# Kernel optimization log

Measured on AMD Instinct MI355X. Metric: run time of the kernel, lower is better.

## Reference

```python
import jax, jax.numpy as jnp
import numpy as np

N_NODES = 100000
N_EDGES = 1600000
IN_DIM = 128
HID_DIM = 64
OUT_DIM = 1


def setup_inputs() -> dict:
    key = jax.random.key(0)
    k = jax.random.split(key, 8)
    x = jax.random.normal(k[0], (N_NODES, IN_DIM), dtype=jnp.float32)
    edge_index = jax.random.randint(k[1], (2, N_EDGES), 0, N_NODES, dtype=jnp.int64)
    # GCNConv layer 1: weight [IN, HID], bias [HID] (glorot-ish scale)
    W1 = jax.random.normal(k[2], (IN_DIM, HID_DIM), dtype=jnp.float32) / np.sqrt(IN_DIM)
    b1 = jnp.zeros((HID_DIM,), dtype=jnp.float32)
    W2 = jax.random.normal(k[3], (HID_DIM, HID_DIM), dtype=jnp.float32) / np.sqrt(HID_DIM)
    b2 = jnp.zeros((HID_DIM,), dtype=jnp.float32)
    Wfc = jax.random.normal(k[4], (HID_DIM, OUT_DIM), dtype=jnp.float32) / np.sqrt(HID_DIM)
    bfc = jnp.zeros((OUT_DIM,), dtype=jnp.float32)
    return {"x": x, "edge_index": edge_index, "W1": W1, "b1": b1,
            "W2": W2, "b2": b2, "Wfc": Wfc, "bfc": bfc}


def _gcn_norm(edge_index, n_nodes):
    # PyG GCNConv default: add self-loops, symmetric normalization.
    src, dst = edge_index[0], edge_index[1]
    loop = jnp.arange(n_nodes, dtype=src.dtype)
    src = jnp.concatenate([src, loop])
    dst = jnp.concatenate([dst, loop])
    deg = jax.ops.segment_sum(jnp.ones_like(dst, dtype=jnp.float32), dst,
                              num_segments=n_nodes)
    deg_isqrt = jax.lax.rsqrt(deg)  # deg >= 1 thanks to self-loops
    norm = deg_isqrt[src] * deg_isqrt[dst]  # [E+N]
    return src, dst, norm


def _gcn_conv(x, src, dst, norm, W, b, n_nodes):
    h = x @ W                      # [N, D_out] dense transform first (D_out <= D_in)
    msg = h[src] * norm[:, None]   # gather + normalize  [E+N, D_out]
    out = jax.ops.segment_sum(msg, dst, num_segments=n_nodes)  # scatter-add
    return out + b


def reference(x, edge_index, W1, b1, W2, b2, Wfc, bfc):
    n = x.shape[0]
    src, dst, norm = _gcn_norm(edge_index, n)
    h = jax.nn.relu(_gcn_conv(x, src, dst, norm, W1, b1, n))
    h = jax.nn.relu(_gcn_conv(h, src, dst, norm, W2, b2, n))
    return h @ Wfc + bfc  # [N, 1]
```

## Files before the change

kernel.cpp:

```cpp
#include <hip/hip_runtime.h>
#include <hip/hip_bf16.h>


#define IN_DIM 128
#define HID 64
#define B1 256
#define MAXNC 128

typedef unsigned int uint;

__device__ inline uint pack_bf16x2(float a, float b) {
    uint ua = __builtin_bit_cast(uint, a);
    uint ub = __builtin_bit_cast(uint, b);
    ua += 0x7fffu + ((ua >> 16) & 1u);
    ub += 0x7fffu + ((ub >> 16) & 1u);
    return (ua >> 16) | (ub & 0xffff0000u);
}
__device__ inline float bf_lo(uint g) { return __builtin_bit_cast(float, g << 16); }
__device__ inline float bf_hi(uint g) { return __builtin_bit_cast(float, g & 0xffff0000u); }

__global__ __launch_bounds__(512) void hist1(const int* __restrict__ dst,
                                             int* __restrict__ ghist,
                                             int E, int NC, int chunk) {
    __shared__ int h[MAXNC];
    int t = threadIdx.x, blk = blockIdx.x;
    if (t < NC) h[t] = 0;
    __syncthreads();
    int s = blk * chunk, e = min(E, s + chunk);
    for (int i = s + t; i < e; i += 512) atomicAdd(&h[dst[i] >> 10], 1);
    __syncthreads();
    if (t < NC) ghist[(size_t)t * B1 + blk] = h[t];
}

__global__ __launch_bounds__(1024) void scan_mat(int* __restrict__ a, int M,
                                                 int* __restrict__ row_off, int N) {
    __shared__ int ws[16], wsoff[16], total_s;
    int t = threadIdx.x;
    int seg = (M + 1023) >> 10;
    int s = t * seg, e = min(M, s + seg);
    int sum = 0;
    for (int i = s; i < e; ++i) sum += a[i];
    int incl = sum;
#pragma unroll
    for (int o = 1; o < 64; o <<= 1) {
        int u = __shfl_up(incl, o, 64);
        if ((t & 63) >= o) incl += u;
    }
    if ((t & 63) == 63) ws[t >> 6] = incl;
    __syncthreads();
    if (t == 0) {
        int run = 0;
#pragma unroll
        for (int i = 0; i < 16; ++i) { wsoff[i] = run; run += ws[i]; }
        total_s = run;
    }
    __syncthreads();
    int run = wsoff[t >> 6] + incl - sum;
    for (int i = s; i < e; ++i) { int tmp = a[i]; a[i] = run; run += tmp; }
    if (t == 0) row_off[N] = total_s;
}

__global__ __launch_bounds__(512) void scatter1(const int* __restrict__ src,
                                                const int* __restrict__ dst,
                                                const int* __restrict__ goff,
                                                uint* __restrict__ pairs,
                                                int E, int NC, int chunk) {
    __shared__ int cur[MAXNC];
    int t = threadIdx.x, blk = blockIdx.x;
    if (t < NC) cur[t] = goff[(size_t)t * B1 + blk];
    __syncthreads();
    int s = blk * chunk, e = min(E, s + chunk);
    for (int i = s + t; i < e; i += 512) {
        int d = dst[i];
        int p = atomicAdd(&cur[d >> 10], 1);
        pairs[p] = ((uint)src[i] << 10) | (uint)(d & 1023);
    }
}

__global__ __launch_bounds__(1024) void build_csr(const uint* __restrict__ pairs,
                                                  const int* __restrict__ goff,
                                                  int* __restrict__ row_off,
                                                  float* __restrict__ disqrt,
                                                  int* __restrict__ col,
                                                  int E, int NC, int N) {
    __shared__ int h[1024], cur[1024];
    __shared__ int ws[16], wsoff[16];
    int b = blockIdx.x, t = threadIdx.x;
    int base = goff[(size_t)b * B1];
    int next = (b + 1 < NC) ? goff[(size_t)(b + 1) * B1] : E;
    h[t] = 0;
    __syncthreads();
    for (int i = base + t; i < next; i += 1024)
        atomicAdd(&h[pairs[i] & 1023u], 1);
    __syncthreads();
    int deg = h[t];
    int incl = deg;
#pragma unroll
    for (int o = 1; o < 64; o <<= 1) {
        int u = __shfl_up(incl, o, 64);
        if ((t & 63) >= o) incl += u;
    }
    if ((t & 63) == 63) ws[t >> 6] = incl;
    __syncthreads();
    if (t == 0) {
        int run = 0;
#pragma unroll
        for (int i = 0; i < 16; ++i) { wsoff[i] = run; run += ws[i]; }
    }
    __syncthreads();
    int excl = wsoff[t >> 6] + incl - deg;
    cur[t] = base + excl;
    int node = (b << 10) + t;
    if (node < N) {
        row_off[node] = base + excl;
        disqrt[node]  = rsqrtf((float)(deg + 1));
    }
    __syncthreads();
    for (int i = base + t; i < next; i += 1024) {
        uint p = pairs[i];
        int pos = atomicAdd(&cur[p & 1023u], 1);
        col[pos] = (int)(p >> 10);
    }
}

template <int K>
__global__ __launch_bounds__(256) void gemm_tile(const float* __restrict__ X,
                                                 const float* __restrict__ W,
                                                 const float* __restrict__ disqrt,
                                                 uint* __restrict__ Tsb, int n) {
    __shared__ float xs[32][68];
    __shared__ float ws[32][64];
    const int tid  = threadIdx.x;
    const int nIdx = tid & 15;
    const int mIdx = tid >> 4;
    const int m0   = blockIdx.x * 64;
    const int r0 = tid >> 3, kq = tid & 7, r1 = r0 + 32;
    const int wk = tid >> 4, wc = tid & 15;
    const int row0 = m0 + r0, row1 = m0 + r1;
    const float4 z4 = make_float4(0.f, 0.f, 0.f, 0.f);

    float4 gx0 = (row0 < n) ? *(const float4*)(X + (size_t)row0 * K + 4 * kq) : z4;
    float4 gx1 = (row1 < n) ? *(const float4*)(X + (size_t)row1 * K + 4 * kq) : z4;
    float4 gw0 = *(const float4*)(W + (size_t)wk * 64 + 4 * wc);
    float4 gw1 = *(const float4*)(W + (size_t)(wk + 16) * 64 + 4 * wc);

    float acc[4][4] = {};
    for (int kc = 0;;) {
        xs[4 * kq + 0][r0] = gx0.x; xs[4 * kq + 1][r0] = gx0.y;
        xs[4 * kq + 2][r0] = gx0.z; xs[4 * kq + 3][r0] = gx0.w;
        xs[4 * kq + 0][r1] = gx1.x; xs[4 * kq + 1][r1] = gx1.y;
        xs[4 * kq + 2][r1] = gx1.z; xs[4 * kq + 3][r1] = gx1.w;
        *(float4*)&ws[wk][4 * wc]      = gw0;
        *(float4*)&ws[wk + 16][4 * wc] = gw1;
        __syncthreads();
        kc += 32;
        const bool more = kc < K;
        if (more) {
            gx0 = (row0 < n) ? *(const float4*)(X + (size_t)row0 * K + kc + 4 * kq) : z4;
            gx1 = (row1 < n) ? *(const float4*)(X + (size_t)row1 * K + kc + 4 * kq) : z4;
            gw0 = *(const float4*)(W + (size_t)(kc + wk) * 64 + 4 * wc);
            gw1 = *(const float4*)(W + (size_t)(kc + wk + 16) * 64 + 4 * wc);
        }
#pragma unroll 8
        for (int k = 0; k < 32; ++k) {
            float4 a = *(const float4*)&xs[k][4 * mIdx];
            float4 b = *(const float4*)&ws[k][4 * nIdx];
            const float* ap = (const float*)&a;
            const float* bp = (const float*)&b;
#pragma unroll
            for (int mi = 0; mi < 4; ++mi)
#pragma unroll
                for (int ni = 0; ni < 4; ++ni)
                    acc[mi][ni] += ap[mi] * bp[ni];
        }
        if (!more) break;
        __syncthreads();
    }
#pragma unroll
    for (int mi = 0; mi < 4; ++mi) {
        int row = m0 + 4 * mIdx + mi;
        if (row < n) {
            float s = disqrt[row];
            uint2 pk;
            pk.x = pack_bf16x2(acc[mi][0] * s, acc[mi][1] * s);
            pk.y = pack_bf16x2(acc[mi][2] * s, acc[mi][3] * s);
            *(uint2*)(Tsb + (size_t)row * 32 + 2 * nIdx) = pk;
        }
    }
}

__global__ __launch_bounds__(256) void gemm_tile_b(const uint* __restrict__ Xb,
                                                   const float* __restrict__ W,
                                                   const float* __restrict__ disqrt,
                                                   uint* __restrict__ Tsb, int n) {
    const int K = 64;
    __shared__ float xs[32][68];
    __shared__ float ws[32][64];
    const int tid  = threadIdx.x;
    const int nIdx = tid & 15;
    const int mIdx = tid >> 4;
    const int m0   = blockIdx.x * 64;
    const int r0 = tid >> 3, kq = tid & 7, r1 = r0 + 32;
    const int wk = tid >> 4, wc = tid & 15;
    const int row0 = m0 + r0, row1 = m0 + r1;
    const uint2 z2 = make_uint2(0u, 0u);

    uint2 gx0 = (row0 < n) ? *(const uint2*)(Xb + (size_t)row0 * 32 + 2 * kq) : z2;
    uint2 gx1 = (row1 < n) ? *(const uint2*)(Xb + (size_t)row1 * 32 + 2 * kq) : z2;
    float4 gw0 = *(const float4*)(W + (size_t)wk * 64 + 4 * wc);
    float4 gw1 = *(const float4*)(W + (size_t)(wk + 16) * 64 + 4 * wc);

    float acc[4][4] = {};
    for (int kc = 0;;) {
        xs[4 * kq + 0][r0] = bf_lo(gx0.x); xs[4 * kq + 1][r0] = bf_hi(gx0.x);
        xs[4 * kq + 2][r0] = bf_lo(gx0.y); xs[4 * kq + 3][r0] = bf_hi(gx0.y);
        xs[4 * kq + 0][r1] = bf_lo(gx1.x); xs[4 * kq + 1][r1] = bf_hi(gx1.x);
        xs[4 * kq + 2][r1] = bf_lo(gx1.y); xs[4 * kq + 3][r1] = bf_hi(gx1.y);
        *(float4*)&ws[wk][4 * wc]      = gw0;
        *(float4*)&ws[wk + 16][4 * wc] = gw1;
        __syncthreads();
        kc += 32;
        const bool more = kc < K;
        if (more) {
            gx0 = (row0 < n) ? *(const uint2*)(Xb + (size_t)row0 * 32 + 16 + 2 * kq) : z2;
            gx1 = (row1 < n) ? *(const uint2*)(Xb + (size_t)row1 * 32 + 16 + 2 * kq) : z2;
            gw0 = *(const float4*)(W + (size_t)(kc + wk) * 64 + 4 * wc);
            gw1 = *(const float4*)(W + (size_t)(kc + wk + 16) * 64 + 4 * wc);
        }
#pragma unroll 8
        for (int k = 0; k < 32; ++k) {
            float4 a = *(const float4*)&xs[k][4 * mIdx];
            float4 b = *(const float4*)&ws[k][4 * nIdx];
            const float* ap = (const float*)&a;
            const float* bp = (const float*)&b;
#pragma unroll
            for (int mi = 0; mi < 4; ++mi)
#pragma unroll
                for (int ni = 0; ni < 4; ++ni)
                    acc[mi][ni] += ap[mi] * bp[ni];
        }
        if (!more) break;
        __syncthreads();
    }
#pragma unroll
    for (int mi = 0; mi < 4; ++mi) {
        int row = m0 + 4 * mIdx + mi;
        if (row < n) {
            float s = disqrt[row];
            uint2 pk;
            pk.x = pack_bf16x2(acc[mi][0] * s, acc[mi][1] * s);
            pk.y = pack_bf16x2(acc[mi][2] * s, acc[mi][3] * s);
            *(uint2*)(Tsb + (size_t)row * 32 + 2 * nIdx) = pk;
        }
    }
}

template <bool FUSE_FC>
__global__ __launch_bounds__(256) void agg_kernel(const uint* __restrict__ Tsb,
                                                  const int* __restrict__ row_off,
                                                  const int* __restrict__ col,
                                                  const float* __restrict__ disqrt,
                                                  const float* __restrict__ bias,
                                                  const float* __restrict__ wfc,
                                                  const float* __restrict__ bfc,
                                                  uint* __restrict__ outb,
                                                  float* __restrict__ outf, int n) {
    int node = blockIdx.x * 4 + (threadIdx.x >> 6);
    if (node >= n) return;
    int lane = threadIdx.x & 63;
    int o = lane >> 3;
    int p = lane & 7;
    float acc[8] = {};
    if (o == 0) {
        uint4 g = *(const uint4*)(Tsb + (size_t)node * 32 + 4 * p);
        acc[0] = bf_lo(g.x); acc[1] = bf_hi(g.x);
        acc[2] = bf_lo(g.y); acc[3] = bf_hi(g.y);
        acc[4] = bf_lo(g.z); acc[5] = bf_hi(g.z);
        acc[6] = bf_lo(g.w); acc[7] = bf_hi(g.w);
    }
    int beg = __builtin_amdgcn_readfirstlane(row_off[node]);
    int end = __builtin_amdgcn_readfirstlane(row_off[node + 1]);
    for (int batch = beg; batch < end; batch += 64) {
        int bn = min(64, end - batch);
        int cv = 0;
        if (batch + lane < end) cv = col[batch + lane];
        int j = 0;
        for (; j + 16 <= bn; j += 16) {
            int s0 = __shfl(cv, j + o, 64);
            int s1 = __shfl(cv, j + 8 + o, 64);
            uint4 g0 = *(const uint4*)(Tsb + (size_t)s0 * 32 + 4 * p);
            uint4 g1 = *(const uint4*)(Tsb + (size_t)s1 * 32 + 4 * p);
            acc[0] += bf_lo(g0.x); acc[1] += bf_hi(g0.x);
            acc[2] += bf_lo(g0.y); acc[3] += bf_hi(g0.y);
            acc[4] += bf_lo(g0.z); acc[5] += bf_hi(g0.z);
            acc[6] += bf_lo(g0.w); acc[7] += bf_hi(g0.w);
            acc[0] += bf_lo(g1.x); acc[1] += bf_hi(g1.x);
            acc[2] += bf_lo(g1.y); acc[3] += bf_hi(g1.y);
            acc[4] += bf_lo(g1.z); acc[5] += bf_hi(g1.z);
            acc[6] += bf_lo(g1.w); acc[7] += bf_hi(g1.w);
        }
        for (; j < bn; j += 8) {
            int idx = j + o;
            int s = __shfl(cv, idx & 63, 64);
            uint4 g = *(const uint4*)(Tsb + (size_t)s * 32 + 4 * p);
            if (idx < bn) {
                acc[0] += bf_lo(g.x); acc[1] += bf_hi(g.x);
                acc[2] += bf_lo(g.y); acc[3] += bf_hi(g.y);
                acc[4] += bf_lo(g.z); acc[5] += bf_hi(g.z);
                acc[6] += bf_lo(g.w); acc[7] += bf_hi(g.w);
            }
        }
    }
#pragma unroll
    for (int k = 0; k < 8; ++k) {
        acc[k] += __shfl_xor(acc[k], 8, 64);
        acc[k] += __shfl_xor(acc[k], 16, 64);
        acc[k] += __shfl_xor(acc[k], 32, 64);
    }
    float dq = disqrt[node];
    float4 bv0 = *(const float4*)(bias + 8 * p);
    float4 bv1 = *(const float4*)(bias + 8 * p + 4);
    float r[8];
    r[0] = fmaxf(acc[0] * dq + bv0.x, 0.f);
    r[1] = fmaxf(acc[1] * dq + bv0.y, 0.f);
    r[2] = fmaxf(acc[2] * dq + bv0.z, 0.f);
    r[3] = fmaxf(acc[3] * dq + bv0.w, 0.f);
    r[4] = fmaxf(acc[4] * dq + bv1.x, 0.f);
    r[5] = fmaxf(acc[5] * dq + bv1.y, 0.f);
    r[6] = fmaxf(acc[6] * dq + bv1.z, 0.f);
    r[7] = fmaxf(acc[7] * dq + bv1.w, 0.f);
    if (!FUSE_FC) {
        if (o == 0) {
            uint4 pk;
            pk.x = pack_bf16x2(r[0], r[1]);
            pk.y = pack_bf16x2(r[2], r[3]);
            pk.z = pack_bf16x2(r[4], r[5]);
            pk.w = pack_bf16x2(r[6], r[7]);
            *(uint4*)(outb + (size_t)node * 32 + 4 * p) = pk;
        }
    } else {
        float4 wv0 = *(const float4*)(wfc + 8 * p);
        float4 wv1 = *(const float4*)(wfc + 8 * p + 4);
        float v = r[0] * wv0.x + r[1] * wv0.y + r[2] * wv0.z + r[3] * wv0.w +
                  r[4] * wv1.x + r[5] * wv1.y + r[6] * wv1.z + r[7] * wv1.w;
        v += __shfl_down(v, 4, 64);
        v += __shfl_down(v, 2, 64);
        v += __shfl_down(v, 1, 64);
        if (lane == 0) outf[node] = v + bfc[0];
    }
}

extern "C" void kernel_launch(void* const* d_in, const int* in_sizes, int n_in,
                              void* d_out, int out_size, void* d_ws, size_t ws_size,
                              hipStream_t stream) {
    const float* x   = (const float*)d_in[0];
    const int*   ei  = (const int*)d_in[1];
    const float* W1  = (const float*)d_in[2];
    const float* b1  = (const float*)d_in[3];
    const float* W2  = (const float*)d_in[4];
    const float* b2  = (const float*)d_in[5];
    const float* Wfc = (const float*)d_in[6];
    const float* bfc = (const float*)d_in[7];
    float* out = (float*)d_out;

    const int N = in_sizes[0] / IN_DIM;
    const int E = in_sizes[1] / 2;
    const int* src = ei;
    const int* dst = ei + E;
    const int NC    = (N + 1023) >> 10;
    const int chunk = (E + B1 - 1) / B1;

    char* w = (char*)d_ws;
    auto alloc = [&](size_t bytes) {
        void* p = (void*)w;
        w += (bytes + 255) & ~(size_t)255;
        return p;
    };
    int*   row_off = (int*)alloc((size_t)(N + 1) * 4);
    float* disqrt  = (float*)alloc((size_t)N * 4);
    int*   goff    = (int*)alloc((size_t)NC * B1 * 4);
    int*   col     = (int*)alloc((size_t)E * 4);
    size_t scrA = (size_t)E * 4, scrB = (size_t)N * HID * 2;
    void*  scr  = alloc(scrA > scrB ? scrA : scrB);
    uint*  h1b  = (uint*)alloc((size_t)N * HID * 2);
    uint*  pairs = (uint*)scr;
    uint*  Tsb   = (uint*)scr;

    hist1<<<B1, 512, 0, stream>>>(dst, goff, E, NC, chunk);
    scan_mat<<<1, 1024, 0, stream>>>(goff, NC * B1, row_off, N);
    scatter1<<<B1, 512, 0, stream>>>(src, dst, goff, pairs, E, NC, chunk);
    build_csr<<<NC, 1024, 0, stream>>>(pairs, goff, row_off, disqrt, col, E, NC, N);

    gemm_tile<IN_DIM><<<(N + 63) / 64, 256, 0, stream>>>(x, W1, disqrt, Tsb, N);
    agg_kernel<false><<<(N + 3) / 4, 256, 0, stream>>>(Tsb, row_off, col, disqrt,
                                                       b1, nullptr, nullptr,
                                                       h1b, nullptr, N);

    gemm_tile_b<<<(N + 63) / 64, 256, 0, stream>>>(h1b, W2, disqrt, Tsb, N);
    agg_kernel<true><<<(N + 3) / 4, 256, 0, stream>>>(Tsb, row_off, col, disqrt,
                                                      b2, Wfc, bfc,
                                                      nullptr, out, N);
}
```

Baseline: 300.1 us.

## Use finer CSR buckets and larger 128-row GEMM tiles

```diff
diff --git a/kernel.cpp b/kernel.cpp
--- a/kernel.cpp
+++ b/kernel.cpp
@@ -5,7 +5,7 @@
 #define IN_DIM 128
 #define HID 64
 #define B1 256
-#define MAXNC 128
+#define MAXNC 512
 
 typedef unsigned int uint;
 
@@ -27,7 +27,7 @@
     if (t < NC) h[t] = 0;
     __syncthreads();
     int s = blk * chunk, e = min(E, s + chunk);
-    for (int i = s + t; i < e; i += 512) atomicAdd(&h[dst[i] >> 10], 1);
+    for (int i = s + t; i < e; i += 512) atomicAdd(&h[dst[i] >> 8], 1);
     __syncthreads();
     if (t < NC) ghist[(size_t)t * B1 + blk] = h[t];
 }
@@ -72,26 +72,26 @@
     int s = blk * chunk, e = min(E, s + chunk);
     for (int i = s + t; i < e; i += 512) {
         int d = dst[i];
-        int p = atomicAdd(&cur[d >> 10], 1);
-        pairs[p] = ((uint)src[i] << 10) | (uint)(d & 1023);
-    }
-}
-
-__global__ __launch_bounds__(1024) void build_csr(const uint* __restrict__ pairs,
-                                                  const int* __restrict__ goff,
-                                                  int* __restrict__ row_off,
-                                                  float* __restrict__ disqrt,
-                                                  int* __restrict__ col,
-                                                  int E, int NC, int N) {
-    __shared__ int h[1024], cur[1024];
-    __shared__ int ws[16], wsoff[16];
+        int p = atomicAdd(&cur[d >> 8], 1);
+        pairs[p] = ((uint)src[i] << 8) | (uint)(d & 255);
+    }
+}
+
+__global__ __launch_bounds__(256) void build_csr(const uint* __restrict__ pairs,
+                                                 const int* __restrict__ goff,
+                                                 int* __restrict__ row_off,
+                                                 float* __restrict__ disqrt,
+                                                 int* __restrict__ col,
+                                                 int E, int NC, int N) {
+    __shared__ int h[256], cur[256];
+    __shared__ int ws[4], wsoff[4];
     int b = blockIdx.x, t = threadIdx.x;
     int base = goff[(size_t)b * B1];
     int next = (b + 1 < NC) ? goff[(size_t)(b + 1) * B1] : E;
     h[t] = 0;
     __syncthreads();
-    for (int i = base + t; i < next; i += 1024)
-        atomicAdd(&h[pairs[i] & 1023u], 1);
+    for (int i = base + t; i < next; i += 256)
+        atomicAdd(&h[pairs[i] & 255u], 1);
     __syncthreads();
     int deg = h[t];
     int incl = deg;
@@ -105,21 +105,21 @@
     if (t == 0) {
         int run = 0;
 #pragma unroll
-        for (int i = 0; i < 16; ++i) { wsoff[i] = run; run += ws[i]; }
+        for (int i = 0; i < 4; ++i) { wsoff[i] = run; run += ws[i]; }
     }
     __syncthreads();
     int excl = wsoff[t >> 6] + incl - deg;
     cur[t] = base + excl;
-    int node = (b << 10) + t;
+    int node = (b << 8) + t;
     if (node < N) {
         row_off[node] = base + excl;
         disqrt[node]  = rsqrtf((float)(deg + 1));
     }
     __syncthreads();
-    for (int i = base + t; i < next; i += 1024) {
+    for (int i = base + t; i < next; i += 256) {
         uint p = pairs[i];
-        int pos = atomicAdd(&cur[p & 1023u], 1);
-        col[pos] = (int)(p >> 10);
+        int pos = atomicAdd(&cur[p & 255u], 1);
+        col[pos] = (int)(p >> 8);
     }
 }
 
@@ -128,63 +128,78 @@
                                                  const float* __restrict__ W,
                                                  const float* __restrict__ disqrt,
                                                  uint* __restrict__ Tsb, int n) {
-    __shared__ float xs[32][68];
+    __shared__ float xs[32][132];
     __shared__ float ws[32][64];
-    const int tid  = threadIdx.x;
-    const int nIdx = tid & 15;
-    const int mIdx = tid >> 4;
-    const int m0   = blockIdx.x * 64;
-    const int r0 = tid >> 3, kq = tid & 7, r1 = r0 + 32;
-    const int wk = tid >> 4, wc = tid & 15;
-    const int row0 = m0 + r0, row1 = m0 + r1;
+    const int tid = threadIdx.x;
+    const int ng  = tid & 15;
+    const int mg  = tid >> 4;
+    const int m0  = blockIdx.x * 128;
     const float4 z4 = make_float4(0.f, 0.f, 0.f, 0.f);
-
-    float4 gx0 = (row0 < n) ? *(const float4*)(X + (size_t)row0 * K + 4 * kq) : z4;
-    float4 gx1 = (row1 < n) ? *(const float4*)(X + (size_t)row1 * K + 4 * kq) : z4;
-    float4 gw0 = *(const float4*)(W + (size_t)wk * 64 + 4 * wc);
-    float4 gw1 = *(const float4*)(W + (size_t)(wk + 16) * 64 + 4 * wc);
-
-    float acc[4][4] = {};
+    int xr[4], xk[4];
+#pragma unroll
+    for (int i = 0; i < 4; ++i) { int f = tid + i * 256; xr[i] = f >> 3; xk[i] = f & 7; }
+    const int wk0 = tid >> 4, wc0 = tid & 15;
+
+    float4 gx[4], gw[2];
+#pragma unroll
+    for (int i = 0; i < 4; ++i) {
+        int row = m0 + xr[i];
+        gx[i] = (row < n) ? *(const float4*)(X + (size_t)row * K + 4 * xk[i]) : z4;
+    }
+    gw[0] = *(const float4*)(W + (size_t)wk0 * 64 + 4 * wc0);
+    gw[1] = *(const float4*)(W + (size_t)(wk0 + 16) * 64 + 4 * wc0);
+
+    float acc[8][4] = {};
     for (int kc = 0;;) {
-        xs[4 * kq + 0][r0] = gx0.x; xs[4 * kq + 1][r0] = gx0.y;
-        xs[4 * kq + 2][r0] = gx0.z; xs[4 * kq + 3][r0] = gx0.w;
-        xs[4 * kq + 0][r1] = gx1.x; xs[4 * kq + 1][r1] = gx1.y;
-        xs[4 * kq + 2][r1] = gx1.z; xs[4 * kq + 3][r1] = gx1.w;
-        *(float4*)&ws[wk][4 * wc]      = gw0;
-        *(float4*)&ws[wk + 16][4 * wc] = gw1;
+#pragma unroll
+        for (int i = 0; i < 4; ++i) {
+            xs[4 * xk[i] + 0][xr[i]] = gx[i].x;
+            xs[4 * xk[i] + 1][xr[i]] = gx[i].y;
+            xs[4 * xk[i] + 2][xr[i]] = gx[i].z;
+            xs[4 * xk[i] + 3][xr[i]] = gx[i].w;
+        }
+        *(float4*)&ws[wk0][4 * wc0]      = gw[0];
+        *(float4*)&ws[wk0 + 16][4 * wc0] = gw[1];
         __syncthreads();
         kc += 32;
         const bool more = kc < K;
         if (more) {
-            gx0 = (row0 < n) ? *(const float4*)(X + (size_t)row0 * K + kc + 4 * kq) : z4;
-            gx1 = (row1 < n) ? *(const float4*)(X + (size_t)row1 * K + kc + 4 * kq) : z4;
-            gw0 = *(const float4*)(W + (size_t)(kc + wk) * 64 + 4 * wc);
-            gw1 = *(const float4*)(W + (size_t)(kc + wk + 16) * 64 + 4 * wc);
-        }
-#pragma unroll 8
+#pragma unroll
+            for (int i = 0; i < 4; ++i) {
+                int row = m0 + xr[i];
+                gx[i] = (row < n) ? *(const float4*)(X + (size_t)row * K + kc + 4 * xk[i]) : z4;
+            }
+            gw[0] = *(const float4*)(W + (size_t)(kc + wk0) * 64 + 4 * wc0);
+            gw[1] = *(const float4*)(W + (size_t)(kc + wk0 + 16) * 64 + 4 * wc0);
+        }
+#pragma unroll 4
         for (int k = 0; k < 32; ++k) {
-            float4 a = *(const float4*)&xs[k][4 * mIdx];
-            float4 b = *(const float4*)&ws[k][4 * nIdx];
-            const float* ap = (const float*)&a;
-            const float* bp = (const float*)&b;
+            float4 a0 = *(const float4*)&xs[k][8 * mg];
+            float4 a1 = *(const float4*)&xs[k][8 * mg + 4];
+            float4 b  = *(const float4*)&ws[k][4 * ng];
+            const float* ap0 = (const float*)&a0;
+            const float* ap1 = (const float*)&a1;
+            const float* bp  = (const float*)&b;
 #pragma unroll
             for (int mi = 0; mi < 4; ++mi)
 #pragma unroll
-                for (int ni = 0; ni < 4; ++ni)
-                    acc[mi][ni] += ap[mi] * bp[ni];
+                for (int ni = 0; ni < 4; ++ni) {
+                    acc[mi][ni]     += ap0[mi] * bp[ni];
+                    acc[mi + 4][ni] += ap1[mi] * bp[ni];
+                }
         }
         if (!more) break;
         __syncthreads();
     }
 #pragma unroll
-    for (int mi = 0; mi < 4; ++mi) {
-        int row = m0 + 4 * mIdx + mi;
+    for (int mi = 0; mi < 8; ++mi) {
+        int row = m0 + 8 * mg + mi;
         if (row < n) {
             float s = disqrt[row];
             uint2 pk;
             pk.x = pack_bf16x2(acc[mi][0] * s, acc[mi][1] * s);
             pk.y = pack_bf16x2(acc[mi][2] * s, acc[mi][3] * s);
-            *(uint2*)(Tsb + (size_t)row * 32 + 2 * nIdx) = pk;
+            *(uint2*)(Tsb + (size_t)row * 32 + 2 * ng) = pk;
         }
     }
 }
@@ -194,63 +209,79 @@
                                                    const float* __restrict__ disqrt,
                                                    uint* __restrict__ Tsb, int n) {
     const int K = 64;
-    __shared__ float xs[32][68];
+    __shared__ float xs[32][132];
     __shared__ float ws[32][64];
-    const int tid  = threadIdx.x;
-    const int nIdx = tid & 15;
-    const int mIdx = tid >> 4;
-    const int m0   = blockIdx.x * 64;
-    const int r0 = tid >> 3, kq = tid & 7, r1 = r0 + 32;
-    const int wk = tid >> 4, wc = tid & 15;
-    const int row0 = m0 + r0, row1 = m0 + r1;
+    const int tid = threadIdx.x;
+    const int ng  = tid & 15;
+    const int mg  = tid >> 4;
+    const int m0  = blockIdx.x * 128;
     const uint2 z2 = make_uint2(0u, 0u);
-
-    uint2 gx0 = (row0 < n) ? *(const uint2*)(Xb + (size_t)row0 * 32 + 2 * kq) : z2;
-    uint2 gx1 = (row1 < n) ? *(const uint2*)(Xb + (size_t)row1 * 32 + 2 * kq) : z2;
-    float4 gw0 = *(const float4*)(W + (size_t)wk * 64 + 4 * wc);
-    float4 gw1 = *(const float4*)(W + (size_t)(wk + 16) * 64 + 4 * wc);
-
-    float acc[4][4] = {};
+    int xr[4], xk[4];
+#pragma unroll
+    for (int i = 0; i < 4; ++i) { int f = tid + i * 256; xr[i] = f >> 3; xk[i] = f & 7; }
+    const int wk0 = tid >> 4, wc0 = tid & 15;
+
+    uint2 gx[4];
+    float4 gw[2];
+#pragma unroll
+    for (int i = 0; i < 4; ++i) {
+        int row = m0 + xr[i];
+        gx[i] = (row < n) ? *(const uint2*)(Xb + (size_t)row * 32 + 2 * xk[i]) : z2;
+    }
+    gw[0] = *(const float4*)(W + (size_t)wk0 * 64 + 4 * wc0);
+    gw[1] = *(const float4*)(W + (size_t)(wk0 + 16) * 64 + 4 * wc0);
+
+    float acc[8][4] = {};
     for (int kc = 0;;) {
-        xs[4 * kq + 0][r0] = bf_lo(gx0.x); xs[4 * kq + 1][r0] = bf_hi(gx0.x);
-        xs[4 * kq + 2][r0] = bf_lo(gx0.y); xs[4 * kq + 3][r0] = bf_hi(gx0.y);
-        xs[4 * kq + 0][r1] = bf_lo(gx1.x); xs[4 * kq + 1][r1] = bf_hi(gx1.x);
-        xs[4 * kq + 2][r1] = bf_lo(gx1.y); xs[4 * kq + 3][r1] = bf_hi(gx1.y);
-        *(float4*)&ws[wk][4 * wc]      = gw0;
-        *(float4*)&ws[wk + 16][4 * wc] = gw1;
+#pragma unroll
+        for (int i = 0; i < 4; ++i) {
+            xs[4 * xk[i] + 0][xr[i]] = bf_lo(gx[i].x);
+            xs[4 * xk[i] + 1][xr[i]] = bf_hi(gx[i].x);
+            xs[4 * xk[i] + 2][xr[i]] = bf_lo(gx[i].y);
+            xs[4 * xk[i] + 3][xr[i]] = bf_hi(gx[i].y);
+        }
+        *(float4*)&ws[wk0][4 * wc0]      = gw[0];
+        *(float4*)&ws[wk0 + 16][4 * wc0] = gw[1];
         __syncthreads();
         kc += 32;
         const bool more = kc < K;
         if (more) {
-            gx0 = (row0 < n) ? *(const uint2*)(Xb + (size_t)row0 * 32 + 16 + 2 * kq) : z2;
-            gx1 = (row1 < n) ? *(const uint2*)(Xb + (size_t)row1 * 32 + 16 + 2 * kq) : z2;
-            gw0 = *(const float4*)(W + (size_t)(kc + wk) * 64 + 4 * wc);
-            gw1 = *(const float4*)(W + (size_t)(kc + wk + 16) * 64 + 4 * wc);
-        }
-#pragma unroll 8
+#pragma unroll
+            for (int i = 0; i < 4; ++i) {
+                int row = m0 + xr[i];
+                gx[i] = (row < n) ? *(const uint2*)(Xb + (size_t)row * 32 + 16 + 2 * xk[i]) : z2;
+            }
+            gw[0] = *(const float4*)(W + (size_t)(kc + wk0) * 64 + 4 * wc0);
+            gw[1] = *(const float4*)(W + (size_t)(kc + wk0 + 16) * 64 + 4 * wc0);
+        }
+#pragma unroll 4
         for (int k = 0; k < 32; ++k) {
-            float4 a = *(const float4*)&xs[k][4 * mIdx];
-            float4 b = *(const float4*)&ws[k][4 * nIdx];
-            const float* ap = (const float*)&a;
-            const float* bp = (const float*)&b;
+            float4 a0 = *(const float4*)&xs[k][8 * mg];
+            float4 a1 = *(const float4*)&xs[k][8 * mg + 4];
+            float4 b  = *(const float4*)&ws[k][4 * ng];
+            const float* ap0 = (const float*)&a0;
+            const float* ap1 = (const float*)&a1;
+            const float* bp  = (const float*)&b;
 #pragma unroll
             for (int mi = 0; mi < 4; ++mi)
 #pragma unroll
-                for (int ni = 0; ni < 4; ++ni)
-                    acc[mi][ni] += ap[mi] * bp[ni];
+                for (int ni = 0; ni < 4; ++ni) {
+                    acc[mi][ni]     += ap0[mi] * bp[ni];
+                    acc[mi + 4][ni] += ap1[mi] * bp[ni];
+                }
         }
         if (!more) break;
         __syncthreads();
     }
 #pragma unroll
-    for (int mi = 0; mi < 4; ++mi) {
-        int row = m0 + 4 * mIdx + mi;
+    for (int mi = 0; mi < 8; ++mi) {
+        int row = m0 + 8 * mg + mi;
         if (row < n) {
             float s = disqrt[row];
             uint2 pk;
             pk.x = pack_bf16x2(acc[mi][0] * s, acc[mi][1] * s);
             pk.y = pack_bf16x2(acc[mi][2] * s, acc[mi][3] * s);
-            *(uint2*)(Tsb + (size_t)row * 32 + 2 * nIdx) = pk;
+            *(uint2*)(Tsb + (size_t)row * 32 + 2 * ng) = pk;
         }
     }
 }
@@ -367,7 +398,7 @@
     const int E = in_sizes[1] / 2;
     const int* src = ei;
     const int* dst = ei + E;
-    const int NC    = (N + 1023) >> 10;
+    const int NC    = (N + 255) >> 8;
     const int chunk = (E + B1 - 1) / B1;
 
     char* w = (char*)d_ws;
@@ -389,14 +420,14 @@
     hist1<<<B1, 512, 0, stream>>>(dst, goff, E, NC, chunk);
     scan_mat<<<1, 1024, 0, stream>>>(goff, NC * B1, row_off, N);
     scatter1<<<B1, 512, 0, stream>>>(src, dst, goff, pairs, E, NC, chunk);
-    build_csr<<<NC, 1024, 0, stream>>>(pairs, goff, row_off, disqrt, col, E, NC, N);
-
-    gemm_tile<IN_DIM><<<(N + 63) / 64, 256, 0, stream>>>(x, W1, disqrt, Tsb, N);
+    build_csr<<<NC, 256, 0, stream>>>(pairs, goff, row_off, disqrt, col, E, NC, N);
+
+    gemm_tile<IN_DIM><<<(N + 127) / 128, 256, 0, stream>>>(x, W1, disqrt, Tsb, N);
     agg_kernel<false><<<(N + 3) / 4, 256, 0, stream>>>(Tsb, row_off, col, disqrt,
                                                        b1, nullptr, nullptr,
                                                        h1b, nullptr, N);
 
-    gemm_tile_b<<<(N + 63) / 64, 256, 0, stream>>>(h1b, W2, disqrt, Tsb, N);
+    gemm_tile_b<<<(N + 127) / 128, 256, 0, stream>>>(h1b, W2, disqrt, Tsb, N);
     agg_kernel<true><<<(N + 3) / 4, 256, 0, stream>>>(Tsb, row_off, col, disqrt,
                                                       b2, Wfc, bfc,
                                                       nullptr, out, N);
```

New measurement: 435.4 us. +45.1%, slower.
